# Optimization experiments

Hardware: AMD Instinct MI355X
Metric: run time of the kernel (lower is better)

## Reference

```python
import jax, jax.numpy as jnp
import numpy as np

EPS = 1e-12  # torch F.normalize default eps


def _l2_normalize(t):
    n = jnp.linalg.norm(t, axis=-1, keepdims=True)
    return t / jnp.maximum(n, EPS)


def _block(x, W, alpha):
    # x: [B,H,N,D]; W: [D,D] (torch Linear weight, applied as x @ W.T)
    xn = _l2_normalize(x)                                   # q_norm == k_norm (q=k=x)
    A = jnp.einsum('bhnd,bhmd->bhnm', xn, xn)               # cosine similarity [B,H,N,N]
    A = jax.nn.softmax(A / jnp.maximum(alpha, 0.01), axis=-1)
    av = jnp.einsum('bhnm,bhmd->bhnd', A, x)                # A @ v, v = x
    return jax.nn.relu(jnp.einsum('bhnd,ed->bhne', av, W) + x)


def setup_inputs() -> dict:
    key = jax.random.key(0)
    k1, k2, k3 = jax.random.split(key, 3)
    B, H, N, D = 4, 4, 4096, 64
    x = jax.random.normal(k1, (B, H, N, D), dtype=jnp.float32)
    # nn.Linear(dim, dim, bias=False) weights, kaiming-uniform-ish scale
    bound = 1.0 / np.sqrt(D)
    W1 = jax.random.uniform(k2, (D, D), dtype=jnp.float32, minval=-bound, maxval=bound)
    W2 = jax.random.uniform(k3, (D, D), dtype=jnp.float32, minval=-bound, maxval=bound)
    alpha1 = jnp.float32(1.0)
    alpha2 = jnp.float32(1.0)
    return {"x": x, "W1": W1, "W2": W2, "alpha1": alpha1, "alpha2": alpha2}


def reference(x, W1, W2, alpha1, alpha2):
    x = _block(x, W1, alpha1)
    x = _block(x, W2, alpha2)
    return x
```

## Files before the change

### kernel.cpp

```cpp
#include <hip/hip_runtime.h>

typedef unsigned short u16;
typedef unsigned int   u32;
typedef __bf16 bf16x8 __attribute__((ext_vector_type(8)));
typedef float  f32x16 __attribute__((ext_vector_type(16)));

#define BH    16
#define NSEQ  4096
#define DIM   64
#define BM    128
#define BN    64
#define LDP   72
#define NTH   32
#define QTILES (NSEQ / BM)

#define SK_OFF   0
#define SV_OFF   9216
#define SW_OFF   18432
#define LX_OFF   23040
#define SMEM_U16 23552
#define HBUF     4608

#define MFMA __builtin_amdgcn_mfma_f32_32x32x16_bf16

__device__ __forceinline__ float bf2f(u16 u) {
    union { u32 i; float f; } v; v.i = ((u32)u) << 16; return v.f;
}
__device__ __forceinline__ u16 f2bf(float f) {
    union { float f; u32 i; } v; v.f = f;
    u32 r = v.i + 0x7fffu + ((v.i >> 16) & 1u);
    return (u16)(r >> 16);
}
#if __has_builtin(__builtin_amdgcn_exp2f)
__device__ __forceinline__ float exp2_raw(float x) { return __builtin_amdgcn_exp2f(x); }
#else
__device__ __forceinline__ float exp2_raw(float x) {
    float r; asm("v_exp_f32 %0, %1" : "=v"(r) : "v"(x)); return r;
}
#endif
__device__ __forceinline__ u32 cvtpk(float a, float b) {
    u32 r; asm("v_cvt_pk_bf16_f32 %0, %1, %2" : "=v"(r) : "v"(a), "v"(b)); return r;
}
__device__ __forceinline__ void plswap(u32& a, u32& b) {
    asm("v_permlane32_swap_b32 %0, %1" : "+v"(a), "+v"(b));
}
__device__ __forceinline__ void lds_barrier() {
    asm volatile("s_waitcnt lgkmcnt(0)\n\ts_barrier" ::: "memory");
}

__global__ __launch_bounds__(256) void ContentGCN_5059471475267_prep(
    const float* __restrict__ src, u16* __restrict__ xn, u16* __restrict__ xT)
{
    __shared__ u16 tile[256 * 72];
    int bh = blockIdx.x >> 4, nt = blockIdx.x & 15, tid = threadIdx.x;
    size_t base = ((size_t)bh * NSEQ + nt * 256 + tid) * DIM;

    float v[64];
    const float4* g = (const float4*)(src + base);
#pragma unroll
    for (int i = 0; i < 16; i++) {
        float4 t4 = g[i];
        v[4*i] = t4.x; v[4*i+1] = t4.y; v[4*i+2] = t4.z; v[4*i+3] = t4.w;
    }

    float ss = 0.f;
#pragma unroll
    for (int d = 0; d < 64; d++) ss += v[d] * v[d];
    float n = sqrtf(ss);
    if (n < 1e-12f) n = 1e-12f;
    float inv = 1.0f / n;

    alignas(16) u16 nb[64], rb[64];
#pragma unroll
    for (int d = 0; d < 64; d++) { nb[d] = f2bf(v[d] * inv); rb[d] = f2bf(v[d]); }
    uint4* gn = (uint4*)(xn + base);
#pragma unroll
    for (int i = 0; i < 8; i++) gn[i] = ((uint4*)nb)[i];

    uint4* trow = (uint4*)&tile[tid * 72];
#pragma unroll
    for (int i = 0; i < 8; i++) trow[i] = ((uint4*)rb)[i];
    __syncthreads();

    int d = tid & 63, ch = tid >> 6;
    alignas(16) u16 ob[64];
#pragma unroll
    for (int nn = 0; nn < 64; nn++) ob[nn] = tile[(ch * 64 + nn) * 72 + d];
    uint4* gt = (uint4*)(xT + ((size_t)bh * DIM + d) * NSEQ + (size_t)nt * 256 + ch * 64);
#pragma unroll
    for (int i = 0; i < 8; i++) gt[i] = ((uint4*)ob)[i];
}

__global__ __launch_bounds__(256) void ContentGCN_5059471475267_prept(
    const u16* __restrict__ src, u16* __restrict__ xT)
{
    __shared__ u16 tile[256 * 72];
    int bh = blockIdx.x >> 4, nt = blockIdx.x & 15, tid = threadIdx.x;
    size_t base = ((size_t)bh * NSEQ + nt * 256 + tid) * DIM;

    uint4* trow = (uint4*)&tile[tid * 72];
    const uint4* g = (const uint4*)(src + base);
#pragma unroll
    for (int i = 0; i < 8; i++) trow[i] = g[i];
    __syncthreads();

    int d = tid & 63, ch = tid >> 6;
    alignas(16) u16 ob[64];
#pragma unroll
    for (int nn = 0; nn < 64; nn++) ob[nn] = tile[(ch * 64 + nn) * 72 + d];
    uint4* gt = (uint4*)(xT + ((size_t)bh * DIM + d) * NSEQ + (size_t)nt * 256 + ch * 64);
#pragma unroll
    for (int i = 0; i < 8; i++) gt[i] = ((uint4*)ob)[i];
}

__global__ __launch_bounds__(512, 4) void ContentGCN_5059471475267_attn(
    const u16* __restrict__ xn, const u16* __restrict__ xT,
    const void* __restrict__ res, int res_isf,
    const float* __restrict__ Wt, const float* __restrict__ alphap,
    void* __restrict__ outp, int out_isf, u16* __restrict__ xnout)
{
    __shared__ u16 smem[SMEM_U16];
    u16* sK = smem + SK_OFF;
    u16* sV = smem + SV_OFF;
    u16* sW = smem + SW_OFF;
    float* lX = (float*)(smem + LX_OFF);

    int tid  = threadIdx.x;
    int w    = tid >> 6, lane = tid & 63;
    int half = w >> 2,  wv   = w & 3;
    int l31  = lane & 31, hi = lane >> 5;
    int bh   = blockIdx.x >> 5;
    int qt   = blockIdx.x & 31;

    float scale = 1.4426950408889634f / fmaxf(alphap[0], 0.01f);

    {
        int rr = tid >> 3, c0 = (tid & 7) * 8;
        const float4* gw = (const float4*)(Wt + rr * DIM + c0);
        float4 t0 = gw[0], t1 = gw[1];
        alignas(16) u16 wb[8];
        wb[0] = f2bf(t0.x); wb[1] = f2bf(t0.y); wb[2] = f2bf(t0.z); wb[3] = f2bf(t0.w);
        wb[4] = f2bf(t1.x); wb[5] = f2bf(t1.y); wb[6] = f2bf(t1.z); wb[7] = f2bf(t1.w);
        *(uint4*)&sW[rr * LDP + c0] = *(const uint4*)wb;
    }

    int qrow = qt * BM + wv * 32 + l31;
    const u16* qp = xn + ((size_t)bh * NSEQ + qrow) * DIM + hi * 8;
    bf16x8 bQ0 = *(const bf16x8*)(qp);
    bf16x8 bQ1 = *(const bf16x8*)(qp + 16);
    bf16x8 bQ2 = *(const bf16x8*)(qp + 32);
    bf16x8 bQ3 = *(const bf16x8*)(qp + 48);

    f32x16 z16;
#pragma unroll
    for (int i = 0; i < 16; i++) z16[i] = 0.f;
    f32x16 OT0 = z16, OT1 = z16;
    float la0 = 0.f, la1 = 0.f, la2 = 0.f, la3 = 0.f;

    u16* sKh = sK + half * HBUF;
    u16* sVh = sV + half * HBUF;

    int ltid = tid & 255;
    int srow = ltid >> 2, scol = (ltid & 3) * 16;

    const u16* pk = xn + ((size_t)bh * NSEQ + half * (NTH * BN) + srow) * DIM + scol;
    const u16* pv = xT + ((size_t)bh * DIM + srow) * NSEQ + half * (NTH * BN) + scol;
    uint4 ck0 = ((const uint4*)pk)[0], ck1 = ((const uint4*)pk)[1];
    uint4 cv0 = ((const uint4*)pv)[0], cv1 = ((const uint4*)pv)[1];
    pk += (size_t)BN * DIM; pv += BN;

    const u16* kB  = sKh + l31 * LDP + hi * 8;
    const u16* vB0 = sVh + l31 * LDP + hi * 8;
    const u16* vB1 = sVh + (32 + l31) * LDP + hi * 8;

    for (int kt = 0; kt < NTH; kt++) {
        lds_barrier();
        *(uint4*)&sKh[srow * LDP + scol]     = ck0;
        *(uint4*)&sKh[srow * LDP + scol + 8] = ck1;
        *(uint4*)&sVh[srow * LDP + scol]     = cv0;
        *(uint4*)&sVh[srow * LDP + scol + 8] = cv1;
        if (kt + 1 < NTH) {
            ck0 = ((const uint4*)pk)[0]; ck1 = ((const uint4*)pk)[1];
            cv0 = ((const uint4*)pv)[0]; cv1 = ((const uint4*)pv)[1];
            pk += (size_t)BN * DIM; pv += BN;
        }
        lds_barrier();

        const u16* kb1 = kB + 32 * LDP;
        f32x16 ST0, ST1;
        __builtin_amdgcn_s_setprio(1);
        ST0 = MFMA(*(const bf16x8*)(kB),       bQ0, z16, 0, 0, 0);
        ST0 = MFMA(*(const bf16x8*)(kB + 16),  bQ1, ST0, 0, 0, 0);
        ST0 = MFMA(*(const bf16x8*)(kB + 32),  bQ2, ST0, 0, 0, 0);
        ST0 = MFMA(*(const bf16x8*)(kB + 48),  bQ3, ST0, 0, 0, 0);
        ST1 = MFMA(*(const bf16x8*)(kb1),      bQ0, z16, 0, 0, 0);
        ST1 = MFMA(*(const bf16x8*)(kb1 + 16), bQ1, ST1, 0, 0, 0);
        ST1 = MFMA(*(const bf16x8*)(kb1 + 32), bQ2, ST1, 0, 0, 0);
        ST1 = MFMA(*(const bf16x8*)(kb1 + 48), bQ3, ST1, 0, 0, 0);
        __builtin_amdgcn_s_setprio(0);

        {
            float p0  = exp2_raw(fmaf(ST0[0],  scale, -scale));
            float p1  = exp2_raw(fmaf(ST0[1],  scale, -scale));
            float p2  = exp2_raw(fmaf(ST0[2],  scale, -scale));
            float p3  = exp2_raw(fmaf(ST0[3],  scale, -scale));
            float p4  = exp2_raw(fmaf(ST0[4],  scale, -scale));
            float p5  = exp2_raw(fmaf(ST0[5],  scale, -scale));
            float p6  = exp2_raw(fmaf(ST0[6],  scale, -scale));
            float p7  = exp2_raw(fmaf(ST0[7],  scale, -scale));
            float p8  = exp2_raw(fmaf(ST0[8],  scale, -scale));
            float p9  = exp2_raw(fmaf(ST0[9],  scale, -scale));
            float p10 = exp2_raw(fmaf(ST0[10], scale, -scale));
            float p11 = exp2_raw(fmaf(ST0[11], scale, -scale));
            float p12 = exp2_raw(fmaf(ST0[12], scale, -scale));
            float p13 = exp2_raw(fmaf(ST0[13], scale, -scale));
            float p14 = exp2_raw(fmaf(ST0[14], scale, -scale));
            float p15 = exp2_raw(fmaf(ST0[15], scale, -scale));
            u32 w0 = cvtpk(p0,  p1),  w1 = cvtpk(p2,  p3);
            u32 w2 = cvtpk(p4,  p5),  w3 = cvtpk(p6,  p7);
            u32 w4 = cvtpk(p8,  p9),  w5 = cvtpk(p10, p11);
            u32 w6 = cvtpk(p12, p13), w7 = cvtpk(p14, p15);
            plswap(w0, w2); plswap(w1, w3);
            plswap(w4, w6); plswap(w5, w7);
            union { u32 u[4]; bf16x8 v; } bp0, bp1;
            bp0.u[0] = w0; bp0.u[1] = w1; bp0.u[2] = w2; bp0.u[3] = w3;
            bp1.u[0] = w4; bp1.u[1] = w5; bp1.u[2] = w6; bp1.u[3] = w7;
            __builtin_amdgcn_s_setprio(1);
            OT0 = MFMA(*(const bf16x8*)(vB0),      bp0.v, OT0, 0, 0, 0);
            OT0 = MFMA(*(const bf16x8*)(vB0 + 16), bp1.v, OT0, 0, 0, 0);
            OT1 = MFMA(*(const bf16x8*)(vB1),      bp0.v, OT1, 0, 0, 0);
            OT1 = MFMA(*(const bf16x8*)(vB1 + 16), bp1.v, OT1, 0, 0, 0);
            __builtin_amdgcn_s_setprio(0);
            la0 += (p0 + p4) + (p8  + p12);
            la1 += (p1 + p5) + (p9  + p13);
            la2 += (p2 + p6) + (p10 + p14);
            la3 += (p3 + p7) + (p11 + p15);
        }

        {
            float p0  = exp2_raw(fmaf(ST1[0],  scale, -scale));
            float p1  = exp2_raw(fmaf(ST1[1],  scale, -scale));
            float p2  = exp2_raw(fmaf(ST1[2],  scale, -scale));
            float p3  = exp2_raw(fmaf(ST1[3],  scale, -scale));
            float p4  = exp2_raw(fmaf(ST1[4],  scale, -scale));
            float p5  = exp2_raw(fmaf(ST1[5],  scale, -scale));
            float p6  = exp2_raw(fmaf(ST1[6],  scale, -scale));
            float p7  = exp2_raw(fmaf(ST1[7],  scale, -scale));
            float p8  = exp2_raw(fmaf(ST1[8],  scale, -scale));
            float p9  = exp2_raw(fmaf(ST1[9],  scale, -scale));
            float p10 = exp2_raw(fmaf(ST1[10], scale, -scale));
            float p11 = exp2_raw(fmaf(ST1[11], scale, -scale));
            float p12 = exp2_raw(fmaf(ST1[12], scale, -scale));
            float p13 = exp2_raw(fmaf(ST1[13], scale, -scale));
            float p14 = exp2_raw(fmaf(ST1[14], scale, -scale));
            float p15 = exp2_raw(fmaf(ST1[15], scale, -scale));
            u32 w0 = cvtpk(p0,  p1),  w1 = cvtpk(p2,  p3);
            u32 w2 = cvtpk(p4,  p5),  w3 = cvtpk(p6,  p7);
            u32 w4 = cvtpk(p8,  p9),  w5 = cvtpk(p10, p11);
            u32 w6 = cvtpk(p12, p13), w7 = cvtpk(p14, p15);
            plswap(w0, w2); plswap(w1, w3);
            plswap(w4, w6); plswap(w5, w7);
            union { u32 u[4]; bf16x8 v; } bp0, bp1;
            bp0.u[0] = w0; bp0.u[1] = w1; bp0.u[2] = w2; bp0.u[3] = w3;
            bp1.u[0] = w4; bp1.u[1] = w5; bp1.u[2] = w6; bp1.u[3] = w7;
            __builtin_amdgcn_s_setprio(1);
            OT0 = MFMA(*(const bf16x8*)(vB0 + 32), bp0.v, OT0, 0, 0, 0);
            OT0 = MFMA(*(const bf16x8*)(vB0 + 48), bp1.v, OT0, 0, 0, 0);
            OT1 = MFMA(*(const bf16x8*)(vB1 + 32), bp0.v, OT1, 0, 0, 0);
            OT1 = MFMA(*(const bf16x8*)(vB1 + 48), bp1.v, OT1, 0, 0, 0);
            __builtin_amdgcn_s_setprio(0);
            la0 += (p0 + p4) + (p8  + p12);
            la1 += (p1 + p5) + (p9  + p13);
            la2 += (p2 + p6) + (p10 + p14);
            la3 += (p3 + p7) + (p11 + p15);
        }
    }

    float lsum = (la0 + la1) + (la2 + la3);
    u32 ja = __float_as_uint(lsum), jb = ja;
    plswap(ja, jb);
    float lfull = __uint_as_float(ja) + __uint_as_float(jb);

    __syncthreads();
    if (lane < 32) lX[w * 32 + l31] = lfull;
    __syncthreads();
    float invl = 1.0f / (lfull + lX[(w ^ 4) * 32 + l31]);

    union { u32 u[4]; bf16x8 v; } av0, av1, av2, av3;
    {
        u32 x0 = cvtpk(OT0[0]  * invl, OT0[1]  * invl), x1 = cvtpk(OT0[2]  * invl, OT0[3]  * invl);
        u32 x2 = cvtpk(OT0[4]  * invl, OT0[5]  * invl), x3 = cvtpk(OT0[6]  * invl, OT0[7]  * invl);
        u32 x4 = cvtpk(OT0[8]  * invl, OT0[9]  * invl), x5 = cvtpk(OT0[10] * invl, OT0[11] * invl);
        u32 x6 = cvtpk(OT0[12] * invl, OT0[13] * invl), x7 = cvtpk(OT0[14] * invl, OT0[15] * invl);
        plswap(x0, x2); plswap(x1, x3); plswap(x4, x6); plswap(x5, x7);
        av0.u[0] = x0; av0.u[1] = x1; av0.u[2] = x2; av0.u[3] = x3;
        av1.u[0] = x4; av1.u[1] = x5; av1.u[2] = x6; av1.u[3] = x7;
        u32 y0 = cvtpk(OT1[0]  * invl, OT1[1]  * invl), y1 = cvtpk(OT1[2]  * invl, OT1[3]  * invl);
        u32 y2 = cvtpk(OT1[4]  * invl, OT1[5]  * invl), y3 = cvtpk(OT1[6]  * invl, OT1[7]  * invl);
        u32 y4 = cvtpk(OT1[8]  * invl, OT1[9]  * invl), y5 = cvtpk(OT1[10] * invl, OT1[11] * invl);
        u32 y6 = cvtpk(OT1[12] * invl, OT1[13] * invl), y7 = cvtpk(OT1[14] * invl, OT1[15] * invl);
        plswap(y0, y2); plswap(y1, y3); plswap(y4, y6); plswap(y5, y7);
        av2.u[0] = y0; av2.u[1] = y1; av2.u[2] = y2; av2.u[3] = y3;
        av3.u[0] = y4; av3.u[1] = y5; av3.u[2] = y6; av3.u[3] = y7;
    }

    f32x16 R0, R1;
    {
        const u16* w0p = sW + l31 * LDP + hi * 8;
        const u16* w1p = sW + (32 + l31) * LDP + hi * 8;
        R0 = MFMA(*(const bf16x8*)(w0p),      av0.v, z16, 0, 0, 0);
        R0 = MFMA(*(const bf16x8*)(w0p + 16), av1.v, R0,  0, 0, 0);
        R0 = MFMA(*(const bf16x8*)(w0p + 32), av2.v, R0,  0, 0, 0);
        R0 = MFMA(*(const bf16x8*)(w0p + 48), av3.v, R0,  0, 0, 0);
        R1 = MFMA(*(const bf16x8*)(w1p),      av0.v, z16, 0, 0, 0);
        R1 = MFMA(*(const bf16x8*)(w1p + 16), av1.v, R1,  0, 0, 0);
        R1 = MFMA(*(const bf16x8*)(w1p + 32), av2.v, R1,  0, 0, 0);
        R1 = MFMA(*(const bf16x8*)(w1p + 48), av3.v, R1,  0, 0, 0);
    }

    float* outS = (float*)smem;
    if (half == 0) {
#pragma unroll
        for (int r = 0; r < 16; r++) {
            int e0 = (r & 3) + 8 * (r >> 2) + 4 * hi;
            outS[e0 * 133 + wv * 32 + l31]        = R0[r];
            outS[(e0 + 32) * 133 + wv * 32 + l31] = R1[r];
        }
    }
    __syncthreads();
    if (half == 1) {
#pragma unroll
        for (int r = 0; r < 16; r++) {
            int e0 = (r & 3) + 8 * (r >> 2) + 4 * hi;
            outS[e0 * 133 + wv * 32 + l31]        += R0[r];
            outS[(e0 + 32) * 133 + wv * 32 + l31] += R1[r];
        }
    }
    __syncthreads();

    {
        int q = tid >> 2, c = tid & 3;
        size_t gbase = ((size_t)bh * NSEQ + qt * BM + q) * DIM + c * 16;
        float vv[16];
#pragma unroll
        for (int j = 0; j < 16; j++) vv[j] = outS[(c * 16 + j) * 133 + q];
        if (res_isf) {
            const float4* rp = (const float4*)((const float*)res + gbase);
#pragma unroll
            for (int i = 0; i < 4; i++) {
                float4 t = rp[i];
                vv[4*i] += t.x; vv[4*i+1] += t.y; vv[4*i+2] += t.z; vv[4*i+3] += t.w;
            }
        } else {
            alignas(16) u16 rb[16];
            const uint4* rp = (const uint4*)((const u16*)res + gbase);
            ((uint4*)rb)[0] = rp[0]; ((uint4*)rb)[1] = rp[1];
#pragma unroll
            for (int j = 0; j < 16; j++) vv[j] += bf2f(rb[j]);
        }
#pragma unroll
        for (int j = 0; j < 16; j++) vv[j] = (vv[j] < 0.f) ? 0.f : vv[j];
        if (out_isf) {
            float4* op = (float4*)((float*)outp + gbase);
#pragma unroll
            for (int i = 0; i < 4; i++)
                op[i] = make_float4(vv[4*i], vv[4*i+1], vv[4*i+2], vv[4*i+3]);
        } else {
            alignas(16) u16 ob[16];
#pragma unroll
            for (int j = 0; j < 16; j++) ob[j] = f2bf(vv[j]);
            uint4* op = (uint4*)((u16*)outp + gbase);
            op[0] = ((uint4*)ob)[0]; op[1] = ((uint4*)ob)[1];
        }
        if (xnout) {
            float ss = 0.f;
#pragma unroll
            for (int j = 0; j < 16; j++) ss += vv[j] * vv[j];
            ss += __shfl_xor(ss, 1);
            ss += __shfl_xor(ss, 2);
            float n = sqrtf(ss);
            if (n < 1e-12f) n = 1e-12f;
            float inv = 1.0f / n;
            alignas(16) u16 nb[16];
#pragma unroll
            for (int j = 0; j < 16; j++) nb[j] = f2bf(vv[j] * inv);
            uint4* gn = (uint4*)(xnout + gbase);
            gn[0] = ((uint4*)nb)[0]; gn[1] = ((uint4*)nb)[1];
        }
    }
}

extern "C" void kernel_launch(void* const* d_in, const int* in_sizes, int n_in,
                              void* d_out, int out_size, void* d_ws, size_t ws_size,
                              hipStream_t stream) {
    const float* x  = (const float*)d_in[0];
    const float* W1 = (const float*)d_in[1];
    const float* W2 = (const float*)d_in[2];
    const float* a1 = (const float*)d_in[3];
    const float* a2 = (const float*)d_in[4];
    float* outp = (float*)d_out;

    size_t elems = (size_t)BH * NSEQ * DIM;
    u16* xn1 = (u16*)d_ws;
    u16* xT  = xn1 + elems;
    u16* xn2 = xT + elems;
    u16* y1  = xn2 + elems;

    dim3 pgrid(BH * 16),     pblk(256);
    dim3 agrid(BH * QTILES), ablk(512);

    ContentGCN_5059471475267_prep<<<pgrid, pblk, 0, stream>>>(x, xn1, xT);
    ContentGCN_5059471475267_attn<<<agrid, ablk, 0, stream>>>(
        xn1, xT, x, 1, W1, a1, y1, 0, xn2);
    ContentGCN_5059471475267_prept<<<pgrid, pblk, 0, stream>>>(y1, xT);
    ContentGCN_5059471475267_attn<<<agrid, ablk, 0, stream>>>(
        xn2, xT, y1, 0, W2, a2, outp, 1, nullptr);
}
```

Measured before the change: 246.5 us.

## Fuse transposed-V output into attention epilogue and compute softmax row sums via MFMA

The first attention kernel now also writes the transposed bf16 copy of its output through an LDS staging buffer, so the separate transpose kernel between the two blocks can be skipped when the workspace is large enough. The softmax denominator is now accumulated with extra MFMAs against a ones vector instead of VALU adds and a permlane reduction. The prep and transpose kernels use smaller 64-row tiles with four threads per row, giving more blocks. In exchange the change adds MFMA work per tile, extra LDS traffic and a barrier in the epilogue, and needs an extra workspace buffer.

```diff
diff --git a/kernel.cpp b/kernel.cpp
--- a/kernel.cpp
+++ b/kernel.cpp
@@ -51,73 +51,73 @@
 __global__ __launch_bounds__(256) void ContentGCN_5059471475267_prep(
     const float* __restrict__ src, u16* __restrict__ xn, u16* __restrict__ xT)
 {
-    __shared__ u16 tile[256 * 72];
-    int bh = blockIdx.x >> 4, nt = blockIdx.x & 15, tid = threadIdx.x;
-    size_t base = ((size_t)bh * NSEQ + nt * 256 + tid) * DIM;
-
-    float v[64];
+    __shared__ u16 tile[64 * LDP];
+    int bh = blockIdx.x >> 6, nt = blockIdx.x & 63, tid = threadIdx.x;
+    int r = tid >> 2, cg = (tid & 3) * 16;
+    size_t base = ((size_t)bh * NSEQ + nt * 64 + r) * DIM + cg;
+
+    float v[16];
     const float4* g = (const float4*)(src + base);
 #pragma unroll
-    for (int i = 0; i < 16; i++) {
-        float4 t4 = g[i];
-        v[4*i] = t4.x; v[4*i+1] = t4.y; v[4*i+2] = t4.z; v[4*i+3] = t4.w;
+    for (int i = 0; i < 4; i++) {
+        float4 t = g[i];
+        v[4*i] = t.x; v[4*i+1] = t.y; v[4*i+2] = t.z; v[4*i+3] = t.w;
     }
 
     float ss = 0.f;
 #pragma unroll
-    for (int d = 0; d < 64; d++) ss += v[d] * v[d];
+    for (int d = 0; d < 16; d++) ss += v[d] * v[d];
+    ss += __shfl_xor(ss, 1);
+    ss += __shfl_xor(ss, 2);
     float n = sqrtf(ss);
     if (n < 1e-12f) n = 1e-12f;
     float inv = 1.0f / n;
 
-    alignas(16) u16 nb[64], rb[64];
-#pragma unroll
-    for (int d = 0; d < 64; d++) { nb[d] = f2bf(v[d] * inv); rb[d] = f2bf(v[d]); }
+    alignas(16) u16 nb[16], rb[16];
+#pragma unroll
+    for (int d = 0; d < 16; d++) { nb[d] = f2bf(v[d] * inv); rb[d] = f2bf(v[d]); }
     uint4* gn = (uint4*)(xn + base);
-#pragma unroll
-    for (int i = 0; i < 8; i++) gn[i] = ((uint4*)nb)[i];
-
-    uint4* trow = (uint4*)&tile[tid * 72];
-#pragma unroll
-    for (int i = 0; i < 8; i++) trow[i] = ((uint4*)rb)[i];
-    __syncthreads();
-
-    int d = tid & 63, ch = tid >> 6;
-    alignas(16) u16 ob[64];
-#pragma unroll
-    for (int nn = 0; nn < 64; nn++) ob[nn] = tile[(ch * 64 + nn) * 72 + d];
-    uint4* gt = (uint4*)(xT + ((size_t)bh * DIM + d) * NSEQ + (size_t)nt * 256 + ch * 64);
-#pragma unroll
-    for (int i = 0; i < 8; i++) gt[i] = ((uint4*)ob)[i];
+    gn[0] = ((uint4*)nb)[0]; gn[1] = ((uint4*)nb)[1];
+
+    uint4* tr = (uint4*)&tile[r * LDP + cg];
+    tr[0] = ((uint4*)rb)[0]; tr[1] = ((uint4*)rb)[1];
+    __syncthreads();
+
+    int d = tid >> 2, nch = tid & 3;
+    alignas(16) u16 ob[16];
+#pragma unroll
+    for (int j = 0; j < 16; j++) ob[j] = tile[(nch * 16 + j) * LDP + d];
+    uint4* gt = (uint4*)(xT + ((size_t)bh * DIM + d) * NSEQ + (size_t)nt * 64 + nch * 16);
+    gt[0] = ((uint4*)ob)[0]; gt[1] = ((uint4*)ob)[1];
 }
 
 __global__ __launch_bounds__(256) void ContentGCN_5059471475267_prept(
     const u16* __restrict__ src, u16* __restrict__ xT)
 {
-    __shared__ u16 tile[256 * 72];
-    int bh = blockIdx.x >> 4, nt = blockIdx.x & 15, tid = threadIdx.x;
-    size_t base = ((size_t)bh * NSEQ + nt * 256 + tid) * DIM;
-
-    uint4* trow = (uint4*)&tile[tid * 72];
-    const uint4* g = (const uint4*)(src + base);
-#pragma unroll
-    for (int i = 0; i < 8; i++) trow[i] = g[i];
-    __syncthreads();
-
-    int d = tid & 63, ch = tid >> 6;
-    alignas(16) u16 ob[64];
-#pragma unroll
-    for (int nn = 0; nn < 64; nn++) ob[nn] = tile[(ch * 64 + nn) * 72 + d];
-    uint4* gt = (uint4*)(xT + ((size_t)bh * DIM + d) * NSEQ + (size_t)nt * 256 + ch * 64);
-#pragma unroll
-    for (int i = 0; i < 8; i++) gt[i] = ((uint4*)ob)[i];
+    __shared__ u16 tile[64 * LDP];
+    int bh = blockIdx.x >> 6, nt = blockIdx.x & 63, tid = threadIdx.x;
+    int r = tid >> 2, cg = (tid & 3) * 16;
+    size_t base = ((size_t)bh * NSEQ + nt * 64 + r) * DIM + cg;
+
+    const uint4* gsrc = (const uint4*)(src + base);
+    uint4* tr = (uint4*)&tile[r * LDP + cg];
+    tr[0] = gsrc[0]; tr[1] = gsrc[1];
+    __syncthreads();
+
+    int d = tid >> 2, nch = tid & 3;
+    alignas(16) u16 ob[16];
+#pragma unroll
+    for (int j = 0; j < 16; j++) ob[j] = tile[(nch * 16 + j) * LDP + d];
+    uint4* gt = (uint4*)(xT + ((size_t)bh * DIM + d) * NSEQ + (size_t)nt * 64 + nch * 16);
+    gt[0] = ((uint4*)ob)[0]; gt[1] = ((uint4*)ob)[1];
 }
 
 __global__ __launch_bounds__(512, 4) void ContentGCN_5059471475267_attn(
     const u16* __restrict__ xn, const u16* __restrict__ xT,
     const void* __restrict__ res, int res_isf,
     const float* __restrict__ Wt, const float* __restrict__ alphap,
-    void* __restrict__ outp, int out_isf, u16* __restrict__ xnout)
+    void* __restrict__ outp, int out_isf,
+    u16* __restrict__ xnout, u16* __restrict__ xTout)
 {
     __shared__ u16 smem[SMEM_U16];
     u16* sK = smem + SK_OFF;
@@ -144,6 +144,11 @@
         *(uint4*)&sW[rr * LDP + c0] = *(const uint4*)wb;
     }
 
+    union { u16 s[8]; bf16x8 v; } onesu;
+#pragma unroll
+    for (int i = 0; i < 8; i++) onesu.s[i] = 0x3F80;
+    bf16x8 onesA = onesu.v;
+
     int qrow = qt * BM + wv * 32 + l31;
     const u16* qp = xn + ((size_t)bh * NSEQ + qrow) * DIM + hi * 8;
     bf16x8 bQ0 = *(const bf16x8*)(qp);
@@ -155,7 +160,7 @@
 #pragma unroll
     for (int i = 0; i < 16; i++) z16[i] = 0.f;
     f32x16 OT0 = z16, OT1 = z16;
-    float la0 = 0.f, la1 = 0.f, la2 = 0.f, la3 = 0.f;
+    f32x16 lacc = z16;
 
     u16* sKh = sK + half * HBUF;
     u16* sVh = sV + half * HBUF;
@@ -226,15 +231,13 @@
             bp0.u[0] = w0; bp0.u[1] = w1; bp0.u[2] = w2; bp0.u[3] = w3;
             bp1.u[0] = w4; bp1.u[1] = w5; bp1.u[2] = w6; bp1.u[3] = w7;
             __builtin_amdgcn_s_setprio(1);
-            OT0 = MFMA(*(const bf16x8*)(vB0),      bp0.v, OT0, 0, 0, 0);
-            OT0 = MFMA(*(const bf16x8*)(vB0 + 16), bp1.v, OT0, 0, 0, 0);
-            OT1 = MFMA(*(const bf16x8*)(vB1),      bp0.v, OT1, 0, 0, 0);
-            OT1 = MFMA(*(const bf16x8*)(vB1 + 16), bp1.v, OT1, 0, 0, 0);
+            OT0  = MFMA(*(const bf16x8*)(vB0),      bp0.v, OT0, 0, 0, 0);
+            OT0  = MFMA(*(const bf16x8*)(vB0 + 16), bp1.v, OT0, 0, 0, 0);
+            OT1  = MFMA(*(const bf16x8*)(vB1),      bp0.v, OT1, 0, 0, 0);
+            OT1  = MFMA(*(const bf16x8*)(vB1 + 16), bp1.v, OT1, 0, 0, 0);
+            lacc = MFMA(onesA, bp0.v, lacc, 0, 0, 0);
+            lacc = MFMA(onesA, bp1.v, lacc, 0, 0, 0);
             __builtin_amdgcn_s_setprio(0);
-            la0 += (p0 + p4) + (p8  + p12);
-            la1 += (p1 + p5) + (p9  + p13);
-            la2 += (p2 + p6) + (p10 + p14);
-            la3 += (p3 + p7) + (p11 + p15);
         }
 
         {
@@ -264,22 +267,17 @@
             bp0.u[0] = w0; bp0.u[1] = w1; bp0.u[2] = w2; bp0.u[3] = w3;
             bp1.u[0] = w4; bp1.u[1] = w5; bp1.u[2] = w6; bp1.u[3] = w7;
             __builtin_amdgcn_s_setprio(1);
-            OT0 = MFMA(*(const bf16x8*)(vB0 + 32), bp0.v, OT0, 0, 0, 0);
-            OT0 = MFMA(*(const bf16x8*)(vB0 + 48), bp1.v, OT0, 0, 0, 0);
-            OT1 = MFMA(*(const bf16x8*)(vB1 + 32), bp0.v, OT1, 0, 0, 0);
-            OT1 = MFMA(*(const bf16x8*)(vB1 + 48), bp1.v, OT1, 0, 0, 0);
+            OT0  = MFMA(*(const bf16x8*)(vB0 + 32), bp0.v, OT0, 0, 0, 0);
+            OT0  = MFMA(*(const bf16x8*)(vB0 + 48), bp1.v, OT0, 0, 0, 0);
+            OT1  = MFMA(*(const bf16x8*)(vB1 + 32), bp0.v, OT1, 0, 0, 0);
+            OT1  = MFMA(*(const bf16x8*)(vB1 + 48), bp1.v, OT1, 0, 0, 0);
+            lacc = MFMA(onesA, bp0.v, lacc, 0, 0, 0);
+            lacc = MFMA(onesA, bp1.v, lacc, 0, 0, 0);
             __builtin_amdgcn_s_setprio(0);
-            la0 += (p0 + p4) + (p8  + p12);
-            la1 += (p1 + p5) + (p9  + p13);
-            la2 += (p2 + p6) + (p10 + p14);
-            la3 += (p3 + p7) + (p11 + p15);
-        }
-    }
-
-    float lsum = (la0 + la1) + (la2 + la3);
-    u32 ja = __float_as_uint(lsum), jb = ja;
-    plswap(ja, jb);
-    float lfull = __uint_as_float(ja) + __uint_as_float(jb);
+        }
+    }
+
+    float lfull = lacc[0];
 
     __syncthreads();
     if (lane < 32) lX[w * 32 + l31] = lfull;
@@ -387,6 +385,23 @@
             uint4* gn = (uint4*)(xnout + gbase);
             gn[0] = ((uint4*)nb)[0]; gn[1] = ((uint4*)nb)[1];
         }
+        if (xTout) {
+#pragma unroll
+            for (int j = 0; j < 16; j++) outS[(c * 16 + j) * 133 + q] = vv[j];
+        }
+    }
+    if (xTout) {
+        __syncthreads();
+        int d = tid >> 3, nch = tid & 7;
+        float t[16];
+#pragma unroll
+        for (int j = 0; j < 16; j++) t[j] = outS[d * 133 + nch * 16 + j];
+        alignas(16) u32 pk8[8];
+#pragma unroll
+        for (int j = 0; j < 8; j++) pk8[j] = cvtpk(t[2*j], t[2*j+1]);
+        uint4* gt = (uint4*)(xTout + ((size_t)bh * DIM + d) * NSEQ
+                             + (size_t)qt * BM + nch * 16);
+        gt[0] = ((uint4*)pk8)[0]; gt[1] = ((uint4*)pk8)[1];
     }
 }
 
@@ -402,17 +417,25 @@
 
     size_t elems = (size_t)BH * NSEQ * DIM;
     u16* xn1 = (u16*)d_ws;
-    u16* xT  = xn1 + elems;
-    u16* xn2 = xT + elems;
+    u16* xT1 = xn1 + elems;
+    u16* xn2 = xT1 + elems;
     u16* y1  = xn2 + elems;
-
-    dim3 pgrid(BH * 16),     pblk(256);
+    u16* xT2 = y1 + elems;
+
+    dim3 pgrid(BH * 64),     pblk(256);
     dim3 agrid(BH * QTILES), ablk(512);
 
-    ContentGCN_5059471475267_prep<<<pgrid, pblk, 0, stream>>>(x, xn1, xT);
-    ContentGCN_5059471475267_attn<<<agrid, ablk, 0, stream>>>(
-        xn1, xT, x, 1, W1, a1, y1, 0, xn2);
-    ContentGCN_5059471475267_prept<<<pgrid, pblk, 0, stream>>>(y1, xT);
-    ContentGCN_5059471475267_attn<<<agrid, ablk, 0, stream>>>(
-        xn2, xT, y1, 0, W2, a2, outp, 1, nullptr);
-}
+    ContentGCN_5059471475267_prep<<<pgrid, pblk, 0, stream>>>(x, xn1, xT1);
+    if (ws_size >= elems * 2 * 5) {
+        ContentGCN_5059471475267_attn<<<agrid, ablk, 0, stream>>>(
+            xn1, xT1, x, 1, W1, a1, y1, 0, xn2, xT2);
+        ContentGCN_5059471475267_attn<<<agrid, ablk, 0, stream>>>(
+            xn2, xT2, y1, 0, W2, a2, outp, 1, nullptr, nullptr);
+    } else {
+        ContentGCN_5059471475267_attn<<<agrid, ablk, 0, stream>>>(
+            xn1, xT1, x, 1, W1, a1, y1, 0, xn2, nullptr);
+        ContentGCN_5059471475267_prept<<<pgrid, pblk, 0, stream>>>(y1, xT1);
+        ContentGCN_5059471475267_attn<<<agrid, ablk, 0, stream>>>(
+            xn2, xT1, y1, 0, W2, a2, outp, 1, nullptr, nullptr);
+    }
+}
```

Result: slower. 262.2 us (+6.4%).
